# Optimization experiments

Measured on AMD Instinct MI355X. Metric: run time of the kernel, lower is better.

The kernel has to match this reference:

```python
import jax, jax.numpy as jnp
import numpy as np

B = 500000
DT = 1.0

def _first_principles_A(dt):
    A = np.eye(8, dtype=np.float32)
    for i in range(4):
        A[i, i + 4] = dt
    return jnp.asarray(A)

def setup_inputs() -> dict:
    key = jax.random.key(0)
    k1, k2 = jax.random.split(key)
    # bbox-like state: keep positions/sizes positive so Q heuristic is sensible
    x = jax.random.uniform(k1, (B, 8, 1), dtype=jnp.float32, minval=0.1, maxval=1.0)
    P = jax.random.normal(k2, (B, 8, 8), dtype=jnp.float32) * 0.1
    A = _first_principles_A(DT)  # relu/triu leave it unchanged but we apply them anyway
    sigma_p = jnp.float32(0.05)
    sigma_v = jnp.float32(0.00625)
    return {"x": x, "P": P, "A": A, "sigma_p": sigma_p, "sigma_v": sigma_v}

def reference(x, P, A, sigma_p, sigma_v):
    # get_motion_matrix: relu then triu
    Ap = jnp.triu(jax.nn.relu(A))  # (8, 8)
    # x_hat = A @ x
    x_hat = jnp.einsum('ij,bjk->bik', Ap, x)  # (B, 8, 1)
    # process-noise heuristic: diag proportional to bbox h, w (x[:,2,0], x[:,3,0])
    h = x[:, 2, 0]
    w = x[:, 3, 0]
    xp, yp = h * sigma_p, w * sigma_p
    xv, yv = h * sigma_v, w * sigma_v
    diag = jnp.stack([xp, yp, xp, yp, xv, yv, xv, yv], axis=-1)  # (B, 8)
    Q = jnp.square(diag)[:, :, None] * jnp.eye(8, dtype=x.dtype)  # (B, 8, 8) diagonal
    # P_hat = A P A^T + Q
    P_hat = jnp.einsum('ij,bjk,lk->bil', Ap, P, Ap) + Q
    return (x_hat, P_hat)
```

## Files before the change

kernel.cpp:

```cpp
#include <hip/hip_runtime.h>


#define ROW_STRIDE 12
#define ELEM_STRIDE 100
#define ELEMS_PER_BLOCK 32

__global__ __launch_bounds__(256) void kalman_predict_kernel(
    const float* __restrict__ x,
    const float* __restrict__ P,
    const float* __restrict__ A,
    const float* __restrict__ sigp_ptr,
    const float* __restrict__ sigv_ptr,
    float* __restrict__ x_hat,
    float* __restrict__ P_hat,
    int B)
{
    __shared__ float lds_m[ELEMS_PER_BLOCK * ELEM_STRIDE];

    float ap[64];
#pragma unroll
    for (int t = 0; t < 64; ++t) {
        float a = fmaxf(A[t], 0.0f);
        if ((t & 7) < (t >> 3)) a = 0.0f;
        ap[t] = __int_as_float(__builtin_amdgcn_readfirstlane(__float_as_int(a)));
    }
    float sigma_p = __int_as_float(__builtin_amdgcn_readfirstlane(__float_as_int(sigp_ptr[0])));
    float sigma_v = __int_as_float(__builtin_amdgcn_readfirstlane(__float_as_int(sigv_ptr[0])));

    int tid = blockIdx.x * blockDim.x + threadIdx.x;
    int e = tid >> 3;
    int r = tid & 7;
    int e_l = threadIdx.x >> 3;

    bool valid = (e < B);
    int e_c = valid ? e : (B - 1);

    const float4* prow = (const float4*)(P + (size_t)e_c * 64 + r * 8);
    float4 pa = prow[0], pb = prow[1];
    float p[8] = {pa.x, pa.y, pa.z, pa.w, pb.x, pb.y, pb.z, pb.w};

    const float4* xrow = (const float4*)(x + (size_t)e_c * 8);
    float4 x0 = xrow[0], x1 = xrow[1];
    float xv[8] = {x0.x, x0.y, x0.z, x0.w, x1.x, x1.y, x1.z, x1.w};

    const float4* arow = (const float4*)(A + r * 8);
    float4 a0 = arow[0], a1 = arow[1];
    float apr[8] = {a0.x, a0.y, a0.z, a0.w, a1.x, a1.y, a1.z, a1.w};
#pragma unroll
    for (int j = 0; j < 8; ++j) {
        float v = fmaxf(apr[j], 0.0f);
        apr[j] = (j >= r) ? v : 0.0f;
    }

    float m[8];
#pragma unroll
    for (int l = 0; l < 8; ++l) {
        float s = 0.0f;
#pragma unroll
        for (int k = 0; k < 8; ++k) s = fmaf(ap[l * 8 + k], p[k], s);
        m[l] = s;
    }

    float* slot = lds_m + e_l * ELEM_STRIDE + r * ROW_STRIDE;
    ((float4*)slot)[0] = make_float4(m[0], m[1], m[2], m[3]);
    ((float4*)(slot + 4))[0] = make_float4(m[4], m[5], m[6], m[7]);

    __syncthreads();

    float hv = (r & 1) ? xv[3] : xv[2];
    float sig = (r < 4) ? sigma_p : sigma_v;
    float q = hv * sig;
    q = q * q;

    float xh = 0.0f;
#pragma unroll
    for (int j = 0; j < 8; ++j) xh = fmaf(apr[j], xv[j], xh);

    float out[8];
#pragma unroll
    for (int l = 0; l < 8; ++l) out[l] = (l == r) ? q : 0.0f;

    const float* ebase = lds_m + e_l * ELEM_STRIDE;
#pragma unroll
    for (int j = 0; j < 8; ++j) {
        const float4* mr = (const float4*)(ebase + j * ROW_STRIDE);
        float4 ma = mr[0], mb = mr[1];
        float mj[8] = {ma.x, ma.y, ma.z, ma.w, mb.x, mb.y, mb.z, mb.w};
#pragma unroll
        for (int l = 0; l < 8; ++l) out[l] = fmaf(apr[j], mj[l], out[l]);
    }

    if (valid) {
        x_hat[(size_t)e * 8 + r] = xh;
        float4* po = (float4*)(P_hat + (size_t)e * 64 + r * 8);
        po[0] = make_float4(out[0], out[1], out[2], out[3]);
        po[1] = make_float4(out[4], out[5], out[6], out[7]);
    }
}

extern "C" void kernel_launch(void* const* d_in, const int* in_sizes, int n_in,
                              void* d_out, int out_size, void* d_ws, size_t ws_size,
                              hipStream_t stream) {
    const float* x  = (const float*)d_in[0];
    const float* P  = (const float*)d_in[1];
    const float* A  = (const float*)d_in[2];
    const float* sp = (const float*)d_in[3];
    const float* sv = (const float*)d_in[4];

    int B = in_sizes[0] / 8;
    float* x_hat = (float*)d_out;
    float* P_hat = (float*)d_out + (size_t)B * 8;

    int threads = B * 8;
    int block = 256;
    int grid = (threads + block - 1) / block;
    kalman_predict_kernel<<<grid, block, 0, stream>>>(x, P, A, sp, sv, x_hat, P_hat, B);
}
```

Baseline: 251.5 us.

## Process two elements per thread and use nontemporal stores for outputs

Result: slower. 258.4 us (+2.8%).

```diff
diff --git a/kernel.cpp b/kernel.cpp
--- a/kernel.cpp
+++ b/kernel.cpp
@@ -3,7 +3,9 @@
 
 #define ROW_STRIDE 12
 #define ELEM_STRIDE 100
-#define ELEMS_PER_BLOCK 32
+#define SLOTS 64
+
+typedef float v4f __attribute__((ext_vector_type(4)));
 
 __global__ __launch_bounds__(256) void kalman_predict_kernel(
     const float* __restrict__ x,
@@ -15,7 +17,7 @@
     float* __restrict__ P_hat,
     int B)
 {
-    __shared__ float lds_m[ELEMS_PER_BLOCK * ELEM_STRIDE];
+    __shared__ float lds_m[SLOTS * ELEM_STRIDE];
 
     float ap[64];
 #pragma unroll
@@ -27,21 +29,15 @@
     float sigma_p = __int_as_float(__builtin_amdgcn_readfirstlane(__float_as_int(sigp_ptr[0])));
     float sigma_v = __int_as_float(__builtin_amdgcn_readfirstlane(__float_as_int(sigv_ptr[0])));
 
-    int tid = blockIdx.x * blockDim.x + threadIdx.x;
-    int e = tid >> 3;
-    int r = tid & 7;
-    int e_l = threadIdx.x >> 3;
-
-    bool valid = (e < B);
-    int e_c = valid ? e : (B - 1);
-
-    const float4* prow = (const float4*)(P + (size_t)e_c * 64 + r * 8);
-    float4 pa = prow[0], pb = prow[1];
-    float p[8] = {pa.x, pa.y, pa.z, pa.w, pb.x, pb.y, pb.z, pb.w};
-
-    const float4* xrow = (const float4*)(x + (size_t)e_c * 8);
-    float4 x0 = xrow[0], x1 = xrow[1];
-    float xv[8] = {x0.x, x0.y, x0.z, x0.w, x1.x, x1.y, x1.z, x1.w};
+    int t = threadIdx.x;
+    int r = t & 7;
+    int s = t >> 3;
+    size_t eb = (size_t)blockIdx.x * 64;
+    size_t e0 = eb + s;
+    size_t e1 = eb + s + 32;
+    bool v0 = e0 < (size_t)B, v1 = e1 < (size_t)B;
+    size_t c0 = v0 ? e0 : (size_t)(B - 1);
+    size_t c1 = v1 ? e1 : (size_t)(B - 1);
 
     const float4* arow = (const float4*)(A + r * 8);
     float4 a0 = arow[0], a1 = arow[1];
@@ -52,49 +48,98 @@
         apr[j] = (j >= r) ? v : 0.0f;
     }
 
-    float m[8];
+    const float4* pr0 = (const float4*)(P + c0 * 64 + r * 8);
+    const float4* pr1 = (const float4*)(P + c1 * 64 + r * 8);
+    float4 p0a = pr0[0], p0b = pr0[1];
+    float4 p1a = pr1[0], p1b = pr1[1];
+    const float4* xr0 = (const float4*)(x + c0 * 8);
+    const float4* xr1 = (const float4*)(x + c1 * 8);
+    float4 x0a = xr0[0], x0b = xr0[1];
+    float4 x1a = xr1[0], x1b = xr1[1];
+
+    float p0[8] = {p0a.x, p0a.y, p0a.z, p0a.w, p0b.x, p0b.y, p0b.z, p0b.w};
+    float p1[8] = {p1a.x, p1a.y, p1a.z, p1a.w, p1b.x, p1b.y, p1b.z, p1b.w};
+    float xv0[8] = {x0a.x, x0a.y, x0a.z, x0a.w, x0b.x, x0b.y, x0b.z, x0b.w};
+    float xv1[8] = {x1a.x, x1a.y, x1a.z, x1a.w, x1b.x, x1b.y, x1b.z, x1b.w};
+
+    float m0[8], m1[8];
 #pragma unroll
     for (int l = 0; l < 8; ++l) {
-        float s = 0.0f;
+        float s0 = 0.0f, s1 = 0.0f;
 #pragma unroll
-        for (int k = 0; k < 8; ++k) s = fmaf(ap[l * 8 + k], p[k], s);
-        m[l] = s;
+        for (int k = 0; k < 8; ++k) {
+            s0 = fmaf(ap[l * 8 + k], p0[k], s0);
+            s1 = fmaf(ap[l * 8 + k], p1[k], s1);
+        }
+        m0[l] = s0; m1[l] = s1;
     }
 
-    float* slot = lds_m + e_l * ELEM_STRIDE + r * ROW_STRIDE;
-    ((float4*)slot)[0] = make_float4(m[0], m[1], m[2], m[3]);
-    ((float4*)(slot + 4))[0] = make_float4(m[4], m[5], m[6], m[7]);
+    float* slot0 = lds_m + (s)      * ELEM_STRIDE + r * ROW_STRIDE;
+    float* slot1 = lds_m + (s + 32) * ELEM_STRIDE + r * ROW_STRIDE;
+    ((float4*)slot0)[0] = make_float4(m0[0], m0[1], m0[2], m0[3]);
+    ((float4*)(slot0 + 4))[0] = make_float4(m0[4], m0[5], m0[6], m0[7]);
+    ((float4*)slot1)[0] = make_float4(m1[0], m1[1], m1[2], m1[3]);
+    ((float4*)(slot1 + 4))[0] = make_float4(m1[4], m1[5], m1[6], m1[7]);
+
+    float xh0 = 0.0f, xh1 = 0.0f;
+#pragma unroll
+    for (int j = 0; j < 8; ++j) {
+        xh0 = fmaf(apr[j], xv0[j], xh0);
+        xh1 = fmaf(apr[j], xv1[j], xh1);
+    }
+    if (v0) __builtin_nontemporal_store(xh0, x_hat + e0 * 8 + r);
+    if (v1) __builtin_nontemporal_store(xh1, x_hat + e1 * 8 + r);
+
+    float sig = (r < 4) ? sigma_p : sigma_v;
+    float hv0 = (r & 1) ? xv0[3] : xv0[2];
+    float hv1 = (r & 1) ? xv1[3] : xv1[2];
+    float q0 = hv0 * sig; q0 *= q0;
+    float q1 = hv1 * sig; q1 *= q1;
 
     __syncthreads();
 
-    float hv = (r & 1) ? xv[3] : xv[2];
-    float sig = (r < 4) ? sigma_p : sigma_v;
-    float q = hv * sig;
-    q = q * q;
-
-    float xh = 0.0f;
+    float out0[8], out1[8];
 #pragma unroll
-    for (int j = 0; j < 8; ++j) xh = fmaf(apr[j], xv[j], xh);
-
-    float out[8];
-#pragma unroll
-    for (int l = 0; l < 8; ++l) out[l] = (l == r) ? q : 0.0f;
-
-    const float* ebase = lds_m + e_l * ELEM_STRIDE;
+    for (int l = 0; l < 8; ++l) {
+        out0[l] = (l == r) ? q0 : 0.0f;
+        out1[l] = (l == r) ? q1 : 0.0f;
+    }
+    const float* eb0 = lds_m + (s)      * ELEM_STRIDE;
+    const float* eb1 = lds_m + (s + 32) * ELEM_STRIDE;
 #pragma unroll
     for (int j = 0; j < 8; ++j) {
-        const float4* mr = (const float4*)(ebase + j * ROW_STRIDE);
-        float4 ma = mr[0], mb = mr[1];
-        float mj[8] = {ma.x, ma.y, ma.z, ma.w, mb.x, mb.y, mb.z, mb.w};
+        float4 ma = ((const float4*)(eb0 + j * ROW_STRIDE))[0];
+        float4 mb = ((const float4*)(eb0 + j * ROW_STRIDE))[1];
+        float aj = apr[j];
+        out0[0] = fmaf(aj, ma.x, out0[0]); out0[1] = fmaf(aj, ma.y, out0[1]);
+        out0[2] = fmaf(aj, ma.z, out0[2]); out0[3] = fmaf(aj, ma.w, out0[3]);
+        out0[4] = fmaf(aj, mb.x, out0[4]); out0[5] = fmaf(aj, mb.y, out0[5]);
+        out0[6] = fmaf(aj, mb.z, out0[6]); out0[7] = fmaf(aj, mb.w, out0[7]);
+    }
 #pragma unroll
-        for (int l = 0; l < 8; ++l) out[l] = fmaf(apr[j], mj[l], out[l]);
+    for (int j = 0; j < 8; ++j) {
+        float4 ma = ((const float4*)(eb1 + j * ROW_STRIDE))[0];
+        float4 mb = ((const float4*)(eb1 + j * ROW_STRIDE))[1];
+        float aj = apr[j];
+        out1[0] = fmaf(aj, ma.x, out1[0]); out1[1] = fmaf(aj, ma.y, out1[1]);
+        out1[2] = fmaf(aj, ma.z, out1[2]); out1[3] = fmaf(aj, ma.w, out1[3]);
+        out1[4] = fmaf(aj, mb.x, out1[4]); out1[5] = fmaf(aj, mb.y, out1[5]);
+        out1[6] = fmaf(aj, mb.z, out1[6]); out1[7] = fmaf(aj, mb.w, out1[7]);
     }
 
-    if (valid) {
-        x_hat[(size_t)e * 8 + r] = xh;
-        float4* po = (float4*)(P_hat + (size_t)e * 64 + r * 8);
-        po[0] = make_float4(out[0], out[1], out[2], out[3]);
-        po[1] = make_float4(out[4], out[5], out[6], out[7]);
+    if (v0) {
+        v4f* po = (v4f*)(P_hat + e0 * 64 + r * 8);
+        v4f lo = {out0[0], out0[1], out0[2], out0[3]};
+        v4f hi = {out0[4], out0[5], out0[6], out0[7]};
+        __builtin_nontemporal_store(lo, po);
+        __builtin_nontemporal_store(hi, po + 1);
+    }
+    if (v1) {
+        v4f* po = (v4f*)(P_hat + e1 * 64 + r * 8);
+        v4f lo = {out1[0], out1[1], out1[2], out1[3]};
+        v4f hi = {out1[4], out1[5], out1[6], out1[7]};
+        __builtin_nontemporal_store(lo, po);
+        __builtin_nontemporal_store(hi, po + 1);
     }
 }
 
@@ -111,8 +156,7 @@
     float* x_hat = (float*)d_out;
     float* P_hat = (float*)d_out + (size_t)B * 8;
 
-    int threads = B * 8;
     int block = 256;
-    int grid = (threads + block - 1) / block;
+    int grid = (B + 63) / 64;
     kalman_predict_kernel<<<grid, block, 0, stream>>>(x, P, A, sp, sv, x_hat, P_hat, B);
 }
```
